# Performance work log

Measured on AMD Instinct MI355X. Metric: run time of the kernel, lower is better.

## Reference

```python
import jax, jax.numpy as jnp
import numpy as np
from jax import lax


def linear_recurrence(decays, impulses):
    """s[t] = decays[t]*s[t-1] + impulses[t], s[-1]=0, via associative scan over axis 0."""
    def comb(e1, e2):
        a1, b1 = e1
        a2, b2 = e2
        return a2 * a1, a2 * b1 + b2
    return lax.associative_scan(comb, (decays, impulses), axis=0)[1]


def setup_inputs() -> dict:
    key = jax.random.key(0)
    ks = jax.random.split(key, 6)
    b, T, d = 16, 1024, 128
    n, m, k = 64, 128, 16
    x = jax.random.normal(ks[0], (b, T, d), jnp.float32)
    R = jax.random.normal(ks[1], (d, k), jnp.float32)               # fixed projection
    theta = jax.random.uniform(ks[2], (k, n // 2), jnp.float32, -np.pi, np.pi)  # eig angles
    C = jax.random.uniform(ks[3], (k, m, n), jnp.float32, -1e-6, 1e-6) / n
    D = jax.random.uniform(ks[4], (k, m), jnp.float32, -1e-3, 1e-3)
    Do = jax.random.uniform(ks[5], (m,), jnp.float32, -1e-7, 1e-7)
    return {"x": x, "R": R, "theta": theta, "C": C, "D": D, "Do": Do}


def _ldstack(x, R, theta, C, D, Do, Delta=2, standard=True):
    c64 = jnp.complex64
    b, T, d = x.shape
    k, half = theta.shape
    n = 2 * half
    m = C.shape[1]
    # (b,T,d) -> (T,b,d) complex, project d -> k
    xc = jnp.transpose(x, (1, 0, 2)).astype(c64) @ R.astype(c64)  # (T,b,k)
    # unitary eigenvalues: lnλ = i*[θ, -θ]
    lnlam = (1j * jnp.concatenate([theta, -theta], axis=1)).astype(c64)  # (k,n)
    lam = jnp.exp(lnlam)
    # B' coefficients (log-space product over eigenvalue ratios, diag excluded)
    eye = jnp.eye(n, dtype=bool)
    ratios = jnp.where(eye[None], 0.0, lam[:, :, None] / lam[:, None, :])  # (k,n,n)
    B = jnp.exp(-jnp.sum(jnp.log(1.0 - ratios), axis=1))                    # (k,n)
    # C' coefficients: C'[k,j,m] = sum_i C[k,m,i] * λ[k,j]^{-(n-i)}
    powers = (n - jnp.arange(1, n + 1)).astype(c64)           # (n,) = [n-1,...,0]
    U = jnp.exp(-powers[None, :, None] * lnlam[:, None, :])   # (k,i,j)
    Cp = jnp.einsum('kmi,kij->kjm', C.astype(c64), U)         # (k,n,m)
    Dc = D.astype(c64)
    Doc = Do.astype(c64)

    alpha = None
    y = None
    for _ in range(Delta):
        Bx = (xc[..., None] * B).reshape(T, b, k * n)          # (T,b,k*n)
        if alpha is None:
            al = jnp.broadcast_to(lam.reshape(1, 1, k * n), (T, b, k * n))
        else:
            al = (alpha * lam).reshape(T, b, k * n)
        if standard:
            z = jnp.zeros((1, b, k * n), c64)
            al = jnp.concatenate([z, al[:-1]], axis=0)
            Bx = jnp.concatenate([z, Bx[:-1]], axis=0)
        s = linear_recurrence(al, Bx).reshape(T, b, k, n)      # (T,b,k,n)
        y = (jnp.einsum('tbkn,knm->tbkm', s, Cp)
             + xc[..., None] * Dc[None, None]
             + Doc)                                            # (T,b,k,m)
        ls = lam[None, None] * s
        alpha = (1.0 / jnp.sqrt(1.0 + jnp.abs(ls) ** 2)).astype(c64)  # recipsq
    y = jnp.mean(y, axis=2).real                               # (T,b,m)
    return jnp.transpose(y, (1, 0, 2))                         # (b,T,m)


def reference(x, R, theta, C, D, Do):
    return _ldstack(x, R, theta, C, D, Do, Delta=2, standard=True)
```

## Files before the change

### kernel.cpp

```cpp
#include <hip/hip_runtime.h>
#include <math.h>

#define TLEN 1024
#define BSZ  16
#define DIN  128
#define KP   16
#define NEIG 64
#define MOUT 128
#define CHUNK_T 256
#define NCHUNK  4

static constexpr size_t XCQ_OFF = 0;
static constexpr size_t LAM_OFF = 262144;
static constexpr size_t BQ_OFF  = 264192;
static constexpr size_t CP_OFF  = 266240;
static constexpr size_t ST_OFF  = 528384;
static constexpr size_t S2_OFF  = 593920;
static constexpr size_t P_OFF   = 8982528;

__device__ __forceinline__ float f32cos(float x) { return (float)cos((double)x); }
__device__ __forceinline__ float f32sin(float x) { return (float)sin((double)x); }

__device__ __forceinline__ float2 cdiv32(float ar, float ai, float cr, float ci) {
  float2 o;
  if (fabsf(ci) <= fabsf(cr)) {
    float rat = __fdiv_rn(ci, cr);
    float scl = __fdiv_rn(1.0f, __fadd_rn(cr, __fmul_rn(ci, rat)));
    o.x = __fmul_rn(__fadd_rn(ar, __fmul_rn(ai, rat)), scl);
    o.y = __fmul_rn(__fsub_rn(ai, __fmul_rn(ar, rat)), scl);
  } else {
    float rat = __fdiv_rn(cr, ci);
    float scl = __fdiv_rn(1.0f, __fadd_rn(ci, __fmul_rn(cr, rat)));
    o.x = __fmul_rn(__fadd_rn(__fmul_rn(ar, rat), ai), scl);
    o.y = __fmul_rn(__fsub_rn(__fmul_rn(ai, rat), ar), scl);
  }
  return o;
}

__global__ __launch_bounds__(256) void k_lam_B(const float* __restrict__ theta,
                        float2* __restrict__ lam, float2* __restrict__ Bq) {
  __shared__ float2 terms[4][64];
  int wid  = threadIdx.x >> 6;
  int lane = threadIdx.x & 63;
  int idx = blockIdx.x * 4 + wid;
  int k = idx >> 6, j = idx & 63;
  float thj = (j < 32) ? theta[k * 32 + j] : -theta[k * 32 + (j - 32)];
  float ljr = f32cos(thj), lji = f32sin(thj);
  float2 tm = make_float2(0.f, 0.f);
  if (lane != j) {
    int i = lane;
    float thi = (i < 32) ? theta[k * 32 + i] : -theta[k * 32 + (i - 32)];
    float lir = f32cos(thi), lii = f32sin(thi);
    float2 r = cdiv32(lir, lii, ljr, lji);
    float tr = __fsub_rn(1.0f, r.x);
    float ti = __fsub_rn(0.0f, r.y);
    double h = sqrt((double)tr * tr + (double)ti * ti);
    tm.x = (float)log(h);
    tm.y = (float)atan2((double)ti, (double)tr);
  }
  terms[wid][lane] = tm;
  __syncthreads();
  if (lane == 0) {
    lam[idx] = make_float2(ljr, lji);
    float sr = 0.f, si = 0.f;
    for (int i = 0; i < NEIG; ++i) {
      sr = __fadd_rn(sr, terms[wid][i].x);
      si = __fadd_rn(si, terms[wid][i].y);
    }
    float er = (float)exp((double)(-sr));
    float cc = f32cos(-si), ss = f32sin(-si);
    Bq[idx] = make_float2(__fmul_rn(er, cc), __fmul_rn(er, ss));
  }
}

__global__ __launch_bounds__(128) void k_Cp(const float* __restrict__ theta,
                     const float* __restrict__ C, float2* __restrict__ Cp) {
  __shared__ float2 sU[64];
  __shared__ float  sC[128][65];
  int tid = threadIdx.x;
  int kj = blockIdx.x;
  int j = kj & 63, k = kj >> 6;
  float lnim = (j < 32) ? theta[k * 32 + j] : -theta[k * 32 + (j - 32)];
  if (tid < 64) {
    int i = tid;
    float p = (float)(63 - i);
    float ph = -__fmul_rn(p, lnim);
    sU[i] = make_float2(f32cos(ph), f32sin(ph));
  }
  const float* Ck = C + ((size_t)k << 13);
  for (int e = tid; e < 128 * 64; e += 128) {
    sC[e >> 6][e & 63] = Ck[e];
  }
  __syncthreads();
  int m = tid;
  float ar = 0.f, ai = 0.f;
  #pragma unroll 8
  for (int i = 0; i < NEIG; ++i) {
    float Cv = sC[m][i];
    float2 U = sU[i];
    ar = __fadd_rn(ar, __fmul_rn(Cv, U.x));
    ai = __fadd_rn(ai, __fmul_rn(Cv, U.y));
  }
  Cp[(size_t)(k * 64 + j) * MOUT + m] = make_float2(ar, ai);
}

__global__ void k_xc(const float* __restrict__ x, const float* __restrict__ R,
                     float* __restrict__ xcq) {
  int idx = blockIdx.x * blockDim.x + threadIdx.x;
  if (idx >= TLEN * BSZ * KP) return;
  int k = idx & 15;
  int b = (idx >> 4) & 15;
  int t = idx >> 8;
  const float4* xr = (const float4*)(x + ((size_t)b * TLEN + t) * DIN);
  double acc = 0.0;
  #pragma unroll 8
  for (int d4 = 0; d4 < DIN / 4; ++d4) {
    float4 v = xr[d4];
    acc = fma((double)v.x, (double)R[(d4 * 4 + 0) * KP + k], acc);
    acc = fma((double)v.y, (double)R[(d4 * 4 + 1) * KP + k], acc);
    acc = fma((double)v.z, (double)R[(d4 * 4 + 2) * KP + k], acc);
    acc = fma((double)v.w, (double)R[(d4 * 4 + 3) * KP + k], acc);
  }
  xcq[idx] = (float)acc;
}

__global__ __launch_bounds__(64) void k_scan(const float2* __restrict__ lam,
                        const float2* __restrict__ Bq,
                        const float* __restrict__ xcq,
                        float2* __restrict__ S2,
                        float* __restrict__ state, int c) {
  __shared__ float sXq[CHUNK_T];
  int j = threadIdx.x;
  int chain = blockIdx.x;
  int b = chain >> 4, k = chain & 15;
  int mode = k * 64 + j;
  int t0 = c * CHUNK_T;
  int tlBeg = (c == 0) ? 1 : 0;
  for (int i = j; i < CHUNK_T; i += 64) {
    int g = t0 + tlBeg - 1 + i;
    sXq[i] = xcq[(size_t)g * (BSZ * KP) + b * KP + k];
  }
  __syncthreads();
  float lr = lam[mode].x, li = lam[mode].y;
  float Br = Bq[mode].x,  Bi = Bq[mode].y;
  float* st = state + (size_t)(chain * 64 + j) * 4;
  float s1r, s1i, s2r, s2i;
  if (c == 0) { s1r = s1i = s2r = s2i = 0.f; }
  else        { s1r = st[0]; s1i = st[1]; s2r = st[2]; s2i = st[3]; }
  float lsr = __fsub_rn(__fmul_rn(lr, s1r), __fmul_rn(li, s1i));
  float lsi = __fadd_rn(__fmul_rn(lr, s1i), __fmul_rn(li, s1r));
  float h  = (float)sqrt((double)lsr * lsr + (double)lsi * lsi);
  float al = __fdiv_rn(1.0f, __fsqrt_rn(__fadd_rn(1.0f, __fmul_rn(h, h))));
  if (c == 0)
    S2[(size_t)(0 * BSZ + b) * 1024 + mode] = make_float2(s2r, s2i);
  #pragma unroll 4
  for (int tl = tlBeg; tl < CHUNK_T; ++tl) {
    float xq = sXq[tl - tlBeg];
    float bxr = __fmul_rn(xq, Br), bxi = __fmul_rn(xq, Bi);
    float a2r = __fmul_rn(al, lr), a2i = __fmul_rn(al, li);
    float t2r = __fsub_rn(__fmul_rn(a2r, s2r), __fmul_rn(a2i, s2i));
    float t2i = __fadd_rn(__fmul_rn(a2r, s2i), __fmul_rn(a2i, s2r));
    s2r = __fadd_rn(t2r, bxr);
    s2i = __fadd_rn(t2i, bxi);
    s1r = __fadd_rn(lsr, bxr);
    s1i = __fadd_rn(lsi, bxi);
    lsr = __fsub_rn(__fmul_rn(lr, s1r), __fmul_rn(li, s1i));
    lsi = __fadd_rn(__fmul_rn(lr, s1i), __fmul_rn(li, s1r));
    h  = (float)sqrt((double)lsr * lsr + (double)lsi * lsi);
    al = __fdiv_rn(1.0f, __fsqrt_rn(__fadd_rn(1.0f, __fmul_rn(h, h))));
    S2[(size_t)(tl * BSZ + b) * 1024 + mode] = make_float2(s2r, s2i);
  }
  st[0] = s1r; st[1] = s1i; st[2] = s2r; st[3] = s2i;
}

__global__ __launch_bounds__(256) void k_y(const float2* __restrict__ S2,
                     const float2* __restrict__ Cp, const float* __restrict__ xcq,
                     const float* __restrict__ D, const float* __restrict__ Dov,
                     float* __restrict__ P, int c) {
  __shared__ __align__(16) float2 sS2[32][66];
  __shared__ __align__(16) float2 sCp[64][66];
  int tid = threadIdx.x;
  int bid = blockIdx.x;
  int kh   = bid >> 8;
  int tile = bid & 255;
  int rowBase = (tile >> 1) * 32;
  int colBase = (tile & 1) * 64;
  int rg = tid & 15;
  int cg = tid >> 4;
  int c0 = cg * 4;
  float msum[2][4] = {};
  int kbeg = kh * 8;
  for (int kk = 0; kk < 8; ++kk) {
    int k = kbeg + kk;
    __syncthreads();
    #pragma unroll
    for (int it = 0; it < 4; ++it) {
      int e = tid + it * 256;
      int r = e >> 5, q = e & 31;
      float4 v = *(const float4*)(S2 + (size_t)(rowBase + r) * 1024 + k * 64 + q * 2);
      *(float4*)&sS2[r][q * 2] = v;
    }
    #pragma unroll
    for (int it = 0; it < 8; ++it) {
      int e = tid + it * 256;
      int n = e >> 5, q = e & 31;
      float4 v = *(const float4*)(Cp + (size_t)(k * 64 + n) * MOUT + colBase + q * 2);
      *(float4*)&sCp[n][q * 2] = v;
    }
    __syncthreads();
    float accn[2][4] = {};
    #pragma unroll 4
    for (int n = 0; n < 64; ++n) {
      float2 sA = sS2[rg][n];
      float2 sB = sS2[rg + 16][n];
      float4 cpA = *(const float4*)&sCp[n][c0];
      float4 cpB = *(const float4*)&sCp[n][c0 + 2];
      float cx[4] = {cpA.x, cpA.z, cpB.x, cpB.z};
      float cy[4] = {cpA.y, cpA.w, cpB.y, cpB.w};
      #pragma unroll
      for (int cc = 0; cc < 4; ++cc) {
        accn[0][cc] = __fadd_rn(accn[0][cc],
            __fsub_rn(__fmul_rn(sA.x, cx[cc]), __fmul_rn(sA.y, cy[cc])));
        accn[1][cc] = __fadd_rn(accn[1][cc],
            __fsub_rn(__fmul_rn(sB.x, cx[cc]), __fmul_rn(sB.y, cy[cc])));
      }
    }
    float4 dA = *(const float4*)(D + k * MOUT + colBase + c0);
    float4 oA = *(const float4*)(Dov + colBase + c0);
    float dv[4] = {dA.x, dA.y, dA.z, dA.w};
    float ov[4] = {oA.x, oA.y, oA.z, oA.w};
    float xv0 = xcq[(size_t)(c * 4096 + rowBase + rg) * KP + k];
    float xv1 = xcq[(size_t)(c * 4096 + rowBase + rg + 16) * KP + k];
    #pragma unroll
    for (int cc = 0; cc < 4; ++cc) {
      float y0 = __fadd_rn(accn[0][cc], __fmul_rn(xv0, dv[cc]));
      float y1 = __fadd_rn(accn[1][cc], __fmul_rn(xv1, dv[cc]));
      y0 = __fadd_rn(y0, ov[cc]);
      y1 = __fadd_rn(y1, ov[cc]);
      msum[0][cc] = __fadd_rn(msum[0][cc], y0);
      msum[1][cc] = __fadd_rn(msum[1][cc], y1);
    }
  }
  #pragma unroll
  for (int rr = 0; rr < 2; ++rr) {
    int r = rowBase + rg + rr * 16;
    float* pp = P + ((size_t)kh * 4096 + r) * MOUT + colBase + c0;
    *(float4*)pp = make_float4(msum[rr][0], msum[rr][1], msum[rr][2], msum[rr][3]);
  }
}

__global__ __launch_bounds__(256) void k_combine(const float* __restrict__ P,
                     float* __restrict__ out, int c) {
  int idx = blockIdx.x * 256 + threadIdx.x;
  int r  = idx >> 5;
  int m4 = (idx & 31) * 4;
  float4 p0 = *(const float4*)(P + (size_t)r * MOUT + m4);
  float4 p1 = *(const float4*)(P + ((size_t)4096 + r) * MOUT + m4);
  int rg = c * 4096 + r;
  int t = rg >> 4, b = rg & 15;
  float4 res;
  res.x = __fdiv_rn(__fadd_rn(p0.x, p1.x), 16.0f);
  res.y = __fdiv_rn(__fadd_rn(p0.y, p1.y), 16.0f);
  res.z = __fdiv_rn(__fadd_rn(p0.z, p1.z), 16.0f);
  res.w = __fdiv_rn(__fadd_rn(p0.w, p1.w), 16.0f);
  *(float4*)(out + ((size_t)b * TLEN + t) * MOUT + m4) = res;
}

extern "C" void kernel_launch(void* const* d_in, const int* in_sizes, int n_in,
                              void* d_out, int out_size, void* d_ws, size_t ws_size,
                              hipStream_t stream) {
  const float* x     = (const float*)d_in[0];
  const float* R     = (const float*)d_in[1];
  const float* theta = (const float*)d_in[2];
  const float* C     = (const float*)d_in[3];
  const float* D     = (const float*)d_in[4];
  const float* Do    = (const float*)d_in[5];
  float* out = (float*)d_out;
  float* ws  = (float*)d_ws;
  float*  xcq = ws + XCQ_OFF;
  float2* lam = (float2*)(ws + LAM_OFF);
  float2* Bq  = (float2*)(ws + BQ_OFF);
  float2* Cp  = (float2*)(ws + CP_OFF);
  float*  st  = ws + ST_OFF;
  float2* S2  = (float2*)(ws + S2_OFF);
  float*  P   = ws + P_OFF;

  hipLaunchKernelGGL(k_lam_B, dim3(256),  dim3(256), 0, stream, theta, lam, Bq);
  hipLaunchKernelGGL(k_Cp,    dim3(1024), dim3(128), 0, stream, theta, C, Cp);
  hipLaunchKernelGGL(k_xc,    dim3(1024), dim3(256), 0, stream, x, R, xcq);
  for (int c = 0; c < NCHUNK; ++c) {
    hipLaunchKernelGGL(k_scan,    dim3(256), dim3(64),  0, stream, lam, Bq, xcq, S2, st, c);
    hipLaunchKernelGGL(k_y,       dim3(512), dim3(256), 0, stream, S2, Cp, xcq, D, Do, P, c);
    hipLaunchKernelGGL(k_combine, dim3(512), dim3(256), 0, stream, P, out, c);
  }
}
```

Before: 408.5 us.

## Retile projection GEMM per eigen-block and stage x/R tiles in shared memory

The output projection kernel now gives each block one k-slice and a 128x128 output tile. It uses 8x8 register blocking over two 32-mode halves, with S2 stored transposed in shared memory, which raises arithmetic intensity per shared-memory load. Per-k partial sums are written to 16 P slices and reduced in the combine kernel instead of 2. The input projection kernel stages x rows and R in shared memory to avoid repeated global reads of R. In exchange, the larger P workspace means more global traffic in the combine step, and the register use per thread rises.

New measurement: 379.8 us. 7.0% less time.

```diff
diff --git a/kernel.cpp b/kernel.cpp
--- a/kernel.cpp
+++ b/kernel.cpp
@@ -104,24 +104,29 @@
   Cp[(size_t)(k * 64 + j) * MOUT + m] = make_float2(ar, ai);
 }
 
-__global__ void k_xc(const float* __restrict__ x, const float* __restrict__ R,
-                     float* __restrict__ xcq) {
-  int idx = blockIdx.x * blockDim.x + threadIdx.x;
-  if (idx >= TLEN * BSZ * KP) return;
-  int k = idx & 15;
-  int b = (idx >> 4) & 15;
-  int t = idx >> 8;
-  const float4* xr = (const float4*)(x + ((size_t)b * TLEN + t) * DIN);
+__global__ __launch_bounds__(256) void k_xc(const float* __restrict__ x,
+                     const float* __restrict__ R, float* __restrict__ xcq) {
+  __shared__ float sX[16][132];
+  __shared__ float sR[128][16];
+  int tid = threadIdx.x;
+  int rBase = blockIdx.x * 16;
+  for (int e = tid; e < DIN * KP; e += 256) sR[e >> 4][e & 15] = R[e];
+  #pragma unroll
+  for (int it = 0; it < 2; ++it) {
+    int e = tid + it * 256;
+    int row = e >> 5, q = e & 31;
+    int g = rBase + row;
+    int t = g >> 4, b = g & 15;
+    float4 v = *(const float4*)(x + ((size_t)b * TLEN + t) * DIN + q * 4);
+    *(float4*)&sX[row][q * 4] = v;
+  }
+  __syncthreads();
+  int r = tid >> 4, k = tid & 15;
   double acc = 0.0;
-  #pragma unroll 8
-  for (int d4 = 0; d4 < DIN / 4; ++d4) {
-    float4 v = xr[d4];
-    acc = fma((double)v.x, (double)R[(d4 * 4 + 0) * KP + k], acc);
-    acc = fma((double)v.y, (double)R[(d4 * 4 + 1) * KP + k], acc);
-    acc = fma((double)v.z, (double)R[(d4 * 4 + 2) * KP + k], acc);
-    acc = fma((double)v.w, (double)R[(d4 * 4 + 3) * KP + k], acc);
-  }
-  xcq[idx] = (float)acc;
+  #pragma unroll 16
+  for (int d = 0; d < DIN; ++d)
+    acc = fma((double)sX[r][d], (double)sR[d][k], acc);
+  xcq[(size_t)(rBase + r) * KP + k] = (float)acc;
 }
 
 __global__ __launch_bounds__(64) void k_scan(const float2* __restrict__ lam,
@@ -173,79 +178,81 @@
   st[0] = s1r; st[1] = s1i; st[2] = s2r; st[3] = s2i;
 }
 
-__global__ __launch_bounds__(256) void k_y(const float2* __restrict__ S2,
+__global__ __launch_bounds__(256, 2) void k_y(const float2* __restrict__ S2,
                      const float2* __restrict__ Cp, const float* __restrict__ xcq,
                      const float* __restrict__ D, const float* __restrict__ Dov,
                      float* __restrict__ P, int c) {
-  __shared__ __align__(16) float2 sS2[32][66];
-  __shared__ __align__(16) float2 sCp[64][66];
+  __shared__ float2 sS2t[32][129];
+  __shared__ float2 sCp[32][128];
   int tid = threadIdx.x;
-  int bid = blockIdx.x;
-  int kh   = bid >> 8;
-  int tile = bid & 255;
-  int rowBase = (tile >> 1) * 32;
-  int colBase = (tile & 1) * 64;
+  int kidx = blockIdx.x >> 5;
+  int rt   = blockIdx.x & 31;
+  int rowBase = rt * 128;
   int rg = tid & 15;
   int cg = tid >> 4;
-  int c0 = cg * 4;
-  float msum[2][4] = {};
-  int kbeg = kh * 8;
-  for (int kk = 0; kk < 8; ++kk) {
-    int k = kbeg + kk;
+  int c0 = cg * 8;
+  float acc[8][8];
+  #pragma unroll
+  for (int jj = 0; jj < 8; ++jj)
+    #pragma unroll
+    for (int q = 0; q < 8; ++q) acc[jj][q] = 0.f;
+
+  #pragma unroll 1
+  for (int nh = 0; nh < 2; ++nh) {
     __syncthreads();
     #pragma unroll
-    for (int it = 0; it < 4; ++it) {
+    for (int it = 0; it < 8; ++it) {
       int e = tid + it * 256;
-      int r = e >> 5, q = e & 31;
-      float4 v = *(const float4*)(S2 + (size_t)(rowBase + r) * 1024 + k * 64 + q * 2);
-      *(float4*)&sS2[r][q * 2] = v;
+      int n2 = (e & 15) * 2;
+      int row = e >> 4;
+      float4 v = *(const float4*)(S2 + (size_t)(rowBase + row) * 1024
+                                     + kidx * 64 + nh * 32 + n2);
+      sS2t[n2][row]     = make_float2(v.x, v.y);
+      sS2t[n2 + 1][row] = make_float2(v.z, v.w);
     }
     #pragma unroll
     for (int it = 0; it < 8; ++it) {
       int e = tid + it * 256;
-      int n = e >> 5, q = e & 31;
-      float4 v = *(const float4*)(Cp + (size_t)(k * 64 + n) * MOUT + colBase + q * 2);
-      *(float4*)&sCp[n][q * 2] = v;
+      int col2 = (e & 63) * 2;
+      int n = e >> 6;
+      float4 v = *(const float4*)(Cp + (size_t)(kidx * 64 + nh * 32 + n) * MOUT + col2);
+      *(float4*)&sCp[n][col2] = v;
     }
     __syncthreads();
-    float accn[2][4] = {};
-    #pragma unroll 4
-    for (int n = 0; n < 64; ++n) {
-      float2 sA = sS2[rg][n];
-      float2 sB = sS2[rg + 16][n];
-      float4 cpA = *(const float4*)&sCp[n][c0];
-      float4 cpB = *(const float4*)&sCp[n][c0 + 2];
-      float cx[4] = {cpA.x, cpA.z, cpB.x, cpB.z};
-      float cy[4] = {cpA.y, cpA.w, cpB.y, cpB.w};
+    #pragma unroll 2
+    for (int n = 0; n < 32; ++n) {
+      float2 a[8];
       #pragma unroll
-      for (int cc = 0; cc < 4; ++cc) {
-        accn[0][cc] = __fadd_rn(accn[0][cc],
-            __fsub_rn(__fmul_rn(sA.x, cx[cc]), __fmul_rn(sA.y, cy[cc])));
-        accn[1][cc] = __fadd_rn(accn[1][cc],
-            __fsub_rn(__fmul_rn(sB.x, cx[cc]), __fmul_rn(sB.y, cy[cc])));
-      }
+      for (int jj = 0; jj < 8; ++jj) a[jj] = sS2t[n][rg + jj * 16];
+      float4 w[4];
+      #pragma unroll
+      for (int q = 0; q < 4; ++q) w[q] = *(const float4*)&sCp[n][c0 + q * 2];
+      float cx[8] = {w[0].x, w[0].z, w[1].x, w[1].z, w[2].x, w[2].z, w[3].x, w[3].z};
+      float cy[8] = {w[0].y, w[0].w, w[1].y, w[1].w, w[2].y, w[2].w, w[3].y, w[3].w};
+      #pragma unroll
+      for (int jj = 0; jj < 8; ++jj)
+        #pragma unroll
+        for (int q = 0; q < 8; ++q)
+          acc[jj][q] = __fadd_rn(acc[jj][q],
+              __fsub_rn(__fmul_rn(a[jj].x, cx[q]), __fmul_rn(a[jj].y, cy[q])));
     }
-    float4 dA = *(const float4*)(D + k * MOUT + colBase + c0);
-    float4 oA = *(const float4*)(Dov + colBase + c0);
-    float dv[4] = {dA.x, dA.y, dA.z, dA.w};
-    float ov[4] = {oA.x, oA.y, oA.z, oA.w};
-    float xv0 = xcq[(size_t)(c * 4096 + rowBase + rg) * KP + k];
-    float xv1 = xcq[(size_t)(c * 4096 + rowBase + rg + 16) * KP + k];
+  }
+  float dv[8], ovv[8];
+  *(float4*)&dv[0]  = *(const float4*)(D + kidx * MOUT + c0);
+  *(float4*)&dv[4]  = *(const float4*)(D + kidx * MOUT + c0 + 4);
+  *(float4*)&ovv[0] = *(const float4*)(Dov + c0);
+  *(float4*)&ovv[4] = *(const float4*)(Dov + c0 + 4);
+  #pragma unroll
+  for (int jj = 0; jj < 8; ++jj) {
+    int row = rowBase + rg + jj * 16;
+    float xv = xcq[(size_t)(c * 4096 + row) * KP + kidx];
+    float res[8];
     #pragma unroll
-    for (int cc = 0; cc < 4; ++cc) {
-      float y0 = __fadd_rn(accn[0][cc], __fmul_rn(xv0, dv[cc]));
-      float y1 = __fadd_rn(accn[1][cc], __fmul_rn(xv1, dv[cc]));
-      y0 = __fadd_rn(y0, ov[cc]);
-      y1 = __fadd_rn(y1, ov[cc]);
-      msum[0][cc] = __fadd_rn(msum[0][cc], y0);
-      msum[1][cc] = __fadd_rn(msum[1][cc], y1);
-    }
-  }
-  #pragma unroll
-  for (int rr = 0; rr < 2; ++rr) {
-    int r = rowBase + rg + rr * 16;
-    float* pp = P + ((size_t)kh * 4096 + r) * MOUT + colBase + c0;
-    *(float4*)pp = make_float4(msum[rr][0], msum[rr][1], msum[rr][2], msum[rr][3]);
+    for (int q = 0; q < 8; ++q)
+      res[q] = __fadd_rn(__fadd_rn(acc[jj][q], __fmul_rn(xv, dv[q])), ovv[q]);
+    float* pp = P + ((size_t)kidx * 4096 + row) * MOUT + c0;
+    *(float4*)pp       = make_float4(res[0], res[1], res[2], res[3]);
+    *(float4*)(pp + 4) = make_float4(res[4], res[5], res[6], res[7]);
   }
 }
 
@@ -254,15 +261,22 @@
   int idx = blockIdx.x * 256 + threadIdx.x;
   int r  = idx >> 5;
   int m4 = (idx & 31) * 4;
-  float4 p0 = *(const float4*)(P + (size_t)r * MOUT + m4);
-  float4 p1 = *(const float4*)(P + ((size_t)4096 + r) * MOUT + m4);
+  float4 s = *(const float4*)(P + (size_t)r * MOUT + m4);
+  #pragma unroll
+  for (int k = 1; k < KP; ++k) {
+    float4 p = *(const float4*)(P + ((size_t)k * 4096 + r) * MOUT + m4);
+    s.x = __fadd_rn(s.x, p.x);
+    s.y = __fadd_rn(s.y, p.y);
+    s.z = __fadd_rn(s.z, p.z);
+    s.w = __fadd_rn(s.w, p.w);
+  }
   int rg = c * 4096 + r;
   int t = rg >> 4, b = rg & 15;
   float4 res;
-  res.x = __fdiv_rn(__fadd_rn(p0.x, p1.x), 16.0f);
-  res.y = __fdiv_rn(__fadd_rn(p0.y, p1.y), 16.0f);
-  res.z = __fdiv_rn(__fadd_rn(p0.z, p1.z), 16.0f);
-  res.w = __fdiv_rn(__fadd_rn(p0.w, p1.w), 16.0f);
+  res.x = __fdiv_rn(s.x, 16.0f);
+  res.y = __fdiv_rn(s.y, 16.0f);
+  res.z = __fdiv_rn(s.z, 16.0f);
+  res.w = __fdiv_rn(s.w, 16.0f);
   *(float4*)(out + ((size_t)b * TLEN + t) * MOUT + m4) = res;
 }
 
```
